# Performance work log

Measured on AMD Instinct MI355X. Metric: run time of the kernel, lower is better.

Reference implementation:

```python
import jax, jax.numpy as jnp
import numpy as np

IN_DIM = 1024
OUT_DIM = 1024
L = 4
HIDDEN = 64
EMB_DIM = 2 + 2 * 2 * L  # 18
BATCH = 8192
W0 = 30.0


def make_embedded_coords():
    gy, gx = jnp.meshgrid(jnp.linspace(-1.0, 1.0, OUT_DIM), jnp.linspace(-1.0, 1.0, IN_DIM), indexing='ij')
    coords = jnp.stack([gy, gx], axis=-1).reshape(-1, 2)  # [rows*cols, 2]
    embeds = [coords]
    for i in range(L):
        freq = 2.0 ** i
        embeds.append(jnp.sin(freq * jnp.pi * coords))
        embeds.append(jnp.cos(freq * jnp.pi * coords))
    return jnp.concatenate(embeds, axis=-1)  # [rows*cols, 18]


def setup_inputs() -> dict:
    key = jax.random.key(0)
    ks = jax.random.split(key, 8)
    # init scales matching torch code
    u = lambda k, shape, b: jax.random.uniform(k, shape, jnp.float32, -b, b)
    W1 = u(ks[0], (HIDDEN, EMB_DIM), 1.0 / EMB_DIM)
    b1 = u(ks[1], (HIDDEN,), 1.0 / np.sqrt(EMB_DIM))
    s2 = np.sqrt(6.0 / HIDDEN) / W0
    W2 = u(ks[2], (HIDDEN, HIDDEN), s2)
    b2 = u(ks[3], (HIDDEN,), 1.0 / np.sqrt(HIDDEN))
    W3 = u(ks[4], (1, HIDDEN), s2)
    b3 = u(ks[5], (1,), 1.0 / np.sqrt(HIDDEN))
    x = jax.random.normal(ks[6], (BATCH, IN_DIM), jnp.float32)
    bias = jnp.zeros((OUT_DIM,), jnp.float32)
    return {
        'x': x,
        'embedded_coords': make_embedded_coords(),
        'W1': W1, 'b1': b1, 'W2': W2, 'b2': b2, 'W3': W3, 'b3': b3,
        'bias': bias,
    }


def reference(x, embedded_coords, W1, b1, W2, b2, W3, b3, bias):
    rows = bias.shape[0]
    cols = x.shape[-1]
    # tiny fully-fused hypernet MLP over rows*cols coordinate points
    h = jnp.sin(W0 * (embedded_coords @ W1.T + b1))  # [rows*cols, 64]
    h = jnp.sin(W0 * (h @ W2.T + b2))                # [rows*cols, 64]
    W = (h @ W3.T + b3).reshape(rows, cols)          # generated weight
    return x @ W.T + bias                            # [batch, out_dim]
```

## Files before the change

kernel.cpp:

```cpp
#include <hip/hip_runtime.h>
#include <hip/hip_bf16.h>


typedef __attribute__((ext_vector_type(8))) short bf16x8;
typedef __attribute__((ext_vector_type(4))) float f32x4;

__device__ __forceinline__ unsigned short f2bf(float f) {
    union { float f; unsigned u; } v; v.f = f;
    unsigned r = v.u + 0x7fffu + ((v.u >> 16) & 1u);
    return (unsigned short)(r >> 16);
}

__device__ __forceinline__ unsigned pktrunc(float a, float b) {
    union { float f; unsigned u; } x, y; x.f = a; y.f = b;
    return (x.u >> 16) | (y.u & 0xffff0000u);
}

__device__ __forceinline__ void async_ld16(const void* g, void* l) {
    __builtin_amdgcn_global_load_lds(
        (__attribute__((address_space(1))) void*)g,
        (__attribute__((address_space(3))) void*)l, 16, 0, 0);
}

__global__ __launch_bounds__(256) void cast_x_kernel(
        const float4* __restrict__ x, unsigned short* __restrict__ xb) {
    long i = (long)blockIdx.x * 256 + threadIdx.x;
    float4 v = x[i];
    ushort4 o;
    o.x = f2bf(v.x); o.y = f2bf(v.y); o.z = f2bf(v.z); o.w = f2bf(v.w);
    *(ushort4*)(xb + i * 4) = o;
}

__global__ __launch_bounds__(256) void siren_tables_kernel(
        const float* __restrict__ ec,
        const float* __restrict__ W1, const float* __restrict__ b1,
        float* __restrict__ Zrow, float* __restrict__ Zcol) {
    int idx = blockIdx.x * 256 + threadIdx.x;
    int j = idx & 63;
    int t = idx >> 6;
    const float* wr = W1 + j * 18;
    if (t < 1024) {
        const float* pe = ec + (long)t * 1024 * 18;
        float z = b1[j];
        #pragma unroll
        for (int i = 0; i < 18; ++i) z += wr[i] * pe[i];
        Zrow[t * 64 + j] = 30.f * z;
    } else {
        int c = t - 1024;
        const float* pe = ec + (long)c * 18;
        float z = 0.f;
        #pragma unroll
        for (int i = 0; i < 18; ++i) z += wr[i] * (pe[i] - ec[i]);
        Zcol[c * 64 + j] = 30.f * z;
    }
}

__global__ __launch_bounds__(256, 4) void siren_w_kernel(
        const float* __restrict__ Zrow, const float* __restrict__ Zcol,
        const float* __restrict__ W2, const float* __restrict__ b2,
        const float* __restrict__ W3, const float* __restrict__ b3,
        unsigned short* __restrict__ Wout) {
    int lane = threadIdx.x & 63;
    int wv   = threadIdx.x >> 6;
    int ln   = lane & 15;
    int kq   = lane >> 4;

    bf16x8 bfrag[2][4];
    #pragma unroll
    for (int kc = 0; kc < 2; ++kc)
        #pragma unroll
        for (int nt = 0; nt < 4; ++nt) {
            const float* src = W2 + (nt * 16 + ln) * 64 + kc * 32 + kq * 8;
            union { bf16x8 v; unsigned u[4]; } tmp;
            #pragma unroll
            for (int q = 0; q < 4; ++q)
                tmp.u[q] = pktrunc(30.f * src[2*q], 30.f * src[2*q + 1]);
            bfrag[kc][nt] = tmp.v;
        }
    float b2v[4], w3v[4];
    #pragma unroll
    for (int nt = 0; nt < 4; ++nt) {
        b2v[nt] = 30.f * b2[nt * 16 + ln];
        w3v[nt] = W3[nt * 16 + ln];
    }
    float b3s = b3[0];

    int wid = blockIdx.x * 4 + wv;
    int r   = wid >> 3;
    int c0  = (wid & 7) * 128;

    const float* zrp = Zrow + (long)r * 64 + kq * 8;
    float zr0[8], zr1[8];
    #pragma unroll
    for (int j = 0; j < 8; ++j) { zr0[j] = zrp[j]; zr1[j] = zrp[32 + j]; }

    for (int it = 0; it < 8; ++it) {
        int c = c0 + it * 16 + ln;
        const float* zc = Zcol + (long)c * 64 + kq * 8;

        float s0[8], s1[8];
        #pragma unroll
        for (int j = 0; j < 8; ++j) {
            s0[j] = __sinf(zr0[j] + zc[j]);
            s1[j] = __sinf(zr1[j] + zc[32 + j]);
        }
        union { bf16x8 v; unsigned u[4]; } a0, a1;
        #pragma unroll
        for (int q = 0; q < 4; ++q) {
            a0.u[q] = pktrunc(s0[2*q], s0[2*q + 1]);
            a1.u[q] = pktrunc(s1[2*q], s1[2*q + 1]);
        }

        f32x4 acc[4] = {};
        #pragma unroll
        for (int nt = 0; nt < 4; ++nt) {
            acc[nt] = __builtin_amdgcn_mfma_f32_16x16x32_bf16(a0.v, bfrag[0][nt], acc[nt], 0, 0, 0);
            acc[nt] = __builtin_amdgcn_mfma_f32_16x16x32_bf16(a1.v, bfrag[1][nt], acc[nt], 0, 0, 0);
        }

        float part[4];
        #pragma unroll
        for (int rg = 0; rg < 4; ++rg) {
            float s = 0.f;
            #pragma unroll
            for (int nt = 0; nt < 4; ++nt)
                s += w3v[nt] * __sinf(acc[nt][rg] + b2v[nt]);
            part[rg] = s;
        }
        #pragma unroll
        for (int m = 1; m < 16; m <<= 1)
            #pragma unroll
            for (int rg = 0; rg < 4; ++rg)
                part[rg] += __shfl_xor(part[rg], m, 64);

        if (ln == 0) {
            long p0 = (long)r * 1024 + c0 + it * 16;
            ushort4 o;
            o.x = f2bf(part[0] + b3s);
            o.y = f2bf(part[1] + b3s);
            o.z = f2bf(part[2] + b3s);
            o.w = f2bf(part[3] + b3s);
            *(ushort4*)(Wout + p0 + kq * 4) = o;
        }
    }
}

__global__ __launch_bounds__(256) void gemm_kernel(
        const unsigned short* __restrict__ A,
        const unsigned short* __restrict__ B,
        const float* __restrict__ bias,
        float* __restrict__ C) {
    const int K = 1024;
    __shared__ __align__(16) unsigned short As[128 * 32];
    __shared__ __align__(16) unsigned short Bs[128 * 32];

    int tid  = threadIdx.x;
    int lane = tid & 63;
    int wv   = tid >> 6;
    int wm   = wv & 1, wn = wv >> 1;
    long Abase = (long)blockIdx.x * 128 * K;
    long Bbase = (long)blockIdx.y * 128 * K;

    int sr = tid >> 2;
    int sc = tid & 3;
    int rsel = lane & 15;
    int csel = lane >> 4;

    f32x4 acc[4][4] = {};

    for (int kt = 0; kt < K; kt += 32) {
        #pragma unroll
        for (int q = 0; q < 2; ++q) {
            int row = q * 64 + sr;
            int cc  = sc ^ ((row >> 1) & 3);
            const unsigned short* ga = A + Abase + (long)row * K + kt + cc * 8;
            const unsigned short* gb = B + Bbase + (long)row * K + kt + cc * 8;
            unsigned short* la = &As[(q * 256 + wv * 64) * 8];
            unsigned short* lb = &Bs[(q * 256 + wv * 64) * 8];
            async_ld16(ga, la);
            async_ld16(gb, lb);
        }
        __syncthreads();

        bf16x8 af[4], bf[4];
        #pragma unroll
        for (int mi = 0; mi < 4; ++mi) {
            int row = wm * 64 + mi * 16 + rsel;
            int ch  = csel ^ ((row >> 1) & 3);
            af[mi] = *(const bf16x8*)&As[row * 32 + ch * 8];
        }
        #pragma unroll
        for (int ni = 0; ni < 4; ++ni) {
            int row = wn * 64 + ni * 16 + rsel;
            int ch  = csel ^ ((row >> 1) & 3);
            bf[ni] = *(const bf16x8*)&Bs[row * 32 + ch * 8];
        }
        #pragma unroll
        for (int mi = 0; mi < 4; ++mi)
            #pragma unroll
            for (int ni = 0; ni < 4; ++ni)
                acc[mi][ni] = __builtin_amdgcn_mfma_f32_16x16x32_bf16(
                    af[mi], bf[ni], acc[mi][ni], 0, 0, 0);
        __syncthreads();
    }

    int row0 = blockIdx.x * 128 + wm * 64;
    int col0 = blockIdx.y * 128 + wn * 64;
    #pragma unroll
    for (int ni = 0; ni < 4; ++ni) {
        int col = col0 + ni * 16 + rsel;
        float bv = bias[col];
        #pragma unroll
        for (int mi = 0; mi < 4; ++mi) {
            int rbase = row0 + mi * 16 + csel * 4;
            #pragma unroll
            for (int r = 0; r < 4; ++r)
                C[(long)(rbase + r) * 1024 + col] = acc[mi][ni][r] + bv;
        }
    }
}

extern "C" void kernel_launch(void* const* d_in, const int* in_sizes, int n_in,
                              void* d_out, int out_size, void* d_ws, size_t ws_size,
                              hipStream_t stream) {
    const float* x    = (const float*)d_in[0];
    const float* ec   = (const float*)d_in[1];
    const float* W1   = (const float*)d_in[2];
    const float* b1   = (const float*)d_in[3];
    const float* W2   = (const float*)d_in[4];
    const float* b2   = (const float*)d_in[5];
    const float* W3   = (const float*)d_in[6];
    const float* b3   = (const float*)d_in[7];
    const float* bias = (const float*)d_in[8];
    float* out = (float*)d_out;

    unsigned short* xb = (unsigned short*)d_ws;
    unsigned short* Wb = xb + (size_t)8192 * 1024;
    float* Zrow = (float*)(Wb + (size_t)1024 * 1024);
    float* Zcol = Zrow + 1024 * 64;

    cast_x_kernel<<<8192, 256, 0, stream>>>((const float4*)x, xb);
    siren_tables_kernel<<<512, 256, 0, stream>>>(ec, W1, b1, Zrow, Zcol);
    siren_w_kernel<<<2048, 256, 0, stream>>>(Zrow, Zcol, W2, b2, W3, b3, Wb);
    dim3 g(64, 8);
    gemm_kernel<<<g, 256, 0, stream>>>(xb, Wb, bias, out);
}
```

Measured before the change: 215.6 us.

## Use native revolution-based sin, double column tiles per wave, swizzle reductions

Pre-scales the SIREN pre-activations by 30/(2π), so the hardware v_sin_f32 (which takes its input in revolutions) can be called directly instead of __sinf with its range reduction. Each wave now processes two 16-column tiles per iteration and 256 columns in total, which halves the grid and interleaves two independent MFMA chains. The 16-lane reduction uses ds_swizzle instead of shfl_xor. Occupancy hint drops from 4 to 3 blocks, and bf16 rounding of the rescaled W2 shifts precision slightly.

```diff
diff --git a/kernel.cpp b/kernel.cpp
--- a/kernel.cpp
+++ b/kernel.cpp
@@ -4,6 +4,8 @@
 
 typedef __attribute__((ext_vector_type(8))) short bf16x8;
 typedef __attribute__((ext_vector_type(4))) float f32x4;
+
+#define SIN_SCALE 4.77464829275686f
 
 __device__ __forceinline__ unsigned short f2bf(float f) {
     union { float f; unsigned u; } v; v.f = f;
@@ -14,6 +16,15 @@
 __device__ __forceinline__ unsigned pktrunc(float a, float b) {
     union { float f; unsigned u; } x, y; x.f = a; y.f = b;
     return (x.u >> 16) | (y.u & 0xffff0000u);
+}
+
+__device__ __forceinline__ float sinrev(float x) {
+    return __builtin_amdgcn_sinf(x);
+}
+
+template <int OFF>
+__device__ __forceinline__ float swz_add(float v) {
+    return v + __int_as_float(__builtin_amdgcn_ds_swizzle(__float_as_int(v), OFF));
 }
 
 __device__ __forceinline__ void async_ld16(const void* g, void* l) {
@@ -44,18 +55,18 @@
         float z = b1[j];
         #pragma unroll
         for (int i = 0; i < 18; ++i) z += wr[i] * pe[i];
-        Zrow[t * 64 + j] = 30.f * z;
+        Zrow[t * 64 + j] = SIN_SCALE * z;
     } else {
         int c = t - 1024;
         const float* pe = ec + (long)c * 18;
         float z = 0.f;
         #pragma unroll
         for (int i = 0; i < 18; ++i) z += wr[i] * (pe[i] - ec[i]);
-        Zcol[c * 64 + j] = 30.f * z;
-    }
-}
-
-__global__ __launch_bounds__(256, 4) void siren_w_kernel(
+        Zcol[c * 64 + j] = SIN_SCALE * z;
+    }
+}
+
+__global__ __launch_bounds__(256, 3) void siren_w_kernel(
         const float* __restrict__ Zrow, const float* __restrict__ Zcol,
         const float* __restrict__ W2, const float* __restrict__ b2,
         const float* __restrict__ W3, const float* __restrict__ b3,
@@ -74,20 +85,20 @@
             union { bf16x8 v; unsigned u[4]; } tmp;
             #pragma unroll
             for (int q = 0; q < 4; ++q)
-                tmp.u[q] = pktrunc(30.f * src[2*q], 30.f * src[2*q + 1]);
+                tmp.u[q] = pktrunc(SIN_SCALE * src[2*q], SIN_SCALE * src[2*q + 1]);
             bfrag[kc][nt] = tmp.v;
         }
     float b2v[4], w3v[4];
     #pragma unroll
     for (int nt = 0; nt < 4; ++nt) {
-        b2v[nt] = 30.f * b2[nt * 16 + ln];
+        b2v[nt] = SIN_SCALE * b2[nt * 16 + ln];
         w3v[nt] = W3[nt * 16 + ln];
     }
     float b3s = b3[0];
 
     int wid = blockIdx.x * 4 + wv;
-    int r   = wid >> 3;
-    int c0  = (wid & 7) * 128;
+    int r   = wid >> 2;
+    int c0  = (wid & 3) * 256;
 
     const float* zrp = Zrow + (long)r * 64 + kq * 8;
     float zr0[8], zr1[8];
@@ -95,52 +106,64 @@
     for (int j = 0; j < 8; ++j) { zr0[j] = zrp[j]; zr1[j] = zrp[32 + j]; }
 
     for (int it = 0; it < 8; ++it) {
-        int c = c0 + it * 16 + ln;
-        const float* zc = Zcol + (long)c * 64 + kq * 8;
-
-        float s0[8], s1[8];
+        int ca = c0 + it * 32 + ln;
+        const float* zca = Zcol + (long)ca * 64 + kq * 8;
+        const float* zcb = zca + 16 * 64;
+
+        float sa0[8], sa1[8], sb0[8], sb1[8];
         #pragma unroll
         for (int j = 0; j < 8; ++j) {
-            s0[j] = __sinf(zr0[j] + zc[j]);
-            s1[j] = __sinf(zr1[j] + zc[32 + j]);
-        }
-        union { bf16x8 v; unsigned u[4]; } a0, a1;
+            sa0[j] = sinrev(zr0[j] + zca[j]);
+            sa1[j] = sinrev(zr1[j] + zca[32 + j]);
+            sb0[j] = sinrev(zr0[j] + zcb[j]);
+            sb1[j] = sinrev(zr1[j] + zcb[32 + j]);
+        }
+        union { bf16x8 v; unsigned u[4]; } a0, a1, bb0, bb1;
         #pragma unroll
         for (int q = 0; q < 4; ++q) {
-            a0.u[q] = pktrunc(s0[2*q], s0[2*q + 1]);
-            a1.u[q] = pktrunc(s1[2*q], s1[2*q + 1]);
-        }
-
-        f32x4 acc[4] = {};
+            a0.u[q]  = pktrunc(sa0[2*q], sa0[2*q + 1]);
+            a1.u[q]  = pktrunc(sa1[2*q], sa1[2*q + 1]);
+            bb0.u[q] = pktrunc(sb0[2*q], sb0[2*q + 1]);
+            bb1.u[q] = pktrunc(sb1[2*q], sb1[2*q + 1]);
+        }
+
+        f32x4 acca[4] = {}, accb[4] = {};
         #pragma unroll
         for (int nt = 0; nt < 4; ++nt) {
-            acc[nt] = __builtin_amdgcn_mfma_f32_16x16x32_bf16(a0.v, bfrag[0][nt], acc[nt], 0, 0, 0);
-            acc[nt] = __builtin_amdgcn_mfma_f32_16x16x32_bf16(a1.v, bfrag[1][nt], acc[nt], 0, 0, 0);
-        }
-
-        float part[4];
+            acca[nt] = __builtin_amdgcn_mfma_f32_16x16x32_bf16(a0.v,  bfrag[0][nt], acca[nt], 0, 0, 0);
+            accb[nt] = __builtin_amdgcn_mfma_f32_16x16x32_bf16(bb0.v, bfrag[0][nt], accb[nt], 0, 0, 0);
+            acca[nt] = __builtin_amdgcn_mfma_f32_16x16x32_bf16(a1.v,  bfrag[1][nt], acca[nt], 0, 0, 0);
+            accb[nt] = __builtin_amdgcn_mfma_f32_16x16x32_bf16(bb1.v, bfrag[1][nt], accb[nt], 0, 0, 0);
+        }
+
+        float pa[4], pb[4];
         #pragma unroll
         for (int rg = 0; rg < 4; ++rg) {
-            float s = 0.f;
-            #pragma unroll
-            for (int nt = 0; nt < 4; ++nt)
-                s += w3v[nt] * __sinf(acc[nt][rg] + b2v[nt]);
-            part[rg] = s;
-        }
-        #pragma unroll
-        for (int m = 1; m < 16; m <<= 1)
-            #pragma unroll
-            for (int rg = 0; rg < 4; ++rg)
-                part[rg] += __shfl_xor(part[rg], m, 64);
+            float s = 0.f, t2 = 0.f;
+            #pragma unroll
+            for (int nt = 0; nt < 4; ++nt) {
+                s  += w3v[nt] * sinrev(acca[nt][rg] + b2v[nt]);
+                t2 += w3v[nt] * sinrev(accb[nt][rg] + b2v[nt]);
+            }
+            pa[rg] = s; pb[rg] = t2;
+        }
+        #pragma unroll
+        for (int rg = 0; rg < 4; ++rg) {
+            pa[rg] = swz_add<0x041F>(pa[rg]);  pb[rg] = swz_add<0x041F>(pb[rg]);
+            pa[rg] = swz_add<0x081F>(pa[rg]);  pb[rg] = swz_add<0x081F>(pb[rg]);
+            pa[rg] = swz_add<0x101F>(pa[rg]);  pb[rg] = swz_add<0x101F>(pb[rg]);
+            pa[rg] = swz_add<0x201F>(pa[rg]);  pb[rg] = swz_add<0x201F>(pb[rg]);
+        }
 
         if (ln == 0) {
-            long p0 = (long)r * 1024 + c0 + it * 16;
-            ushort4 o;
-            o.x = f2bf(part[0] + b3s);
-            o.y = f2bf(part[1] + b3s);
-            o.z = f2bf(part[2] + b3s);
-            o.w = f2bf(part[3] + b3s);
-            *(ushort4*)(Wout + p0 + kq * 4) = o;
+            long p0 = (long)r * 1024 + c0 + it * 32;
+            ushort4 oa, ob;
+            oa.x = f2bf(pa[0] + b3s); oa.y = f2bf(pa[1] + b3s);
+            oa.z = f2bf(pa[2] + b3s); oa.w = f2bf(pa[3] + b3s);
+            ob.x = f2bf(pb[0] + b3s); ob.y = f2bf(pb[1] + b3s);
+            ob.z = f2bf(pb[2] + b3s); ob.w = f2bf(pb[3] + b3s);
+            *(ushort4*)(Wout + p0 + kq * 4)      = oa;
+            *(ushort4*)(Wout + p0 + 16 + kq * 4) = ob;
         }
     }
 }
@@ -241,7 +264,7 @@
 
     cast_x_kernel<<<8192, 256, 0, stream>>>((const float4*)x, xb);
     siren_tables_kernel<<<512, 256, 0, stream>>>(ec, W1, b1, Zrow, Zcol);
-    siren_w_kernel<<<2048, 256, 0, stream>>>(Zrow, Zcol, W2, b2, W3, b3, Wb);
+    siren_w_kernel<<<1024, 256, 0, stream>>>(Zrow, Zcol, W2, b2, W3, b3, Wb);
     dim3 g(64, 8);
     gemm_kernel<<<g, 256, 0, stream>>>(xb, Wb, bias, out);
 }
```

Result: faster. 209.6 us (-2.8%).
